# Kernel tuning notes

Hardware: AMD Instinct MI355X
Metric: run time of the kernel (lower is better)

## Reference

```python
import jax, jax.numpy as jnp
import numpy as np

N = 50000      # nodes
E = 640000     # edges
D = 128        # hidden_dim (tower in_dim, towers=1)
DE = 64        # edge_hidden_dim
L = 2          # propagation_depth
AVG_D = 3.5    # avg_d scaler constant
EPS = 1e-5


def setup_inputs() -> dict:
    key = jax.random.key(0)
    ks = jax.random.split(key, 8)
    h = jax.random.normal(ks[0], (N, D), jnp.float32)
    e = jax.random.normal(ks[1], (E, DE), jnp.float32)
    src = jax.random.randint(ks[2], (E,), 0, N, jnp.int32)
    dst = jax.random.randint(ks[3], (E,), 0, N, jnp.int32)
    pre_in = 2 * D + DE            # cat([h_src, h_dst, e])
    post_in = (4 * 3 + 1) * D      # (n_agg * n_scalers + 1) * in_dim
    pre_W = jax.random.normal(ks[4], (L, pre_in, D), jnp.float32) * 0.05
    pre_b = jnp.zeros((L, D), jnp.float32)
    post_W = jax.random.normal(ks[5], (L, post_in, D), jnp.float32) * 0.02
    post_b = jnp.zeros((L, D), jnp.float32)
    mix_W = jax.random.normal(ks[6], (L, D, D), jnp.float32) * 0.05
    mix_b = jnp.zeros((L, D), jnp.float32)
    return {"h": h, "e": e, "src": src, "dst": dst,
            "pre_W": pre_W, "pre_b": pre_b,
            "post_W": post_W, "post_b": post_b,
            "mix_W": mix_W, "mix_b": mix_b}


def reference(h, e, src, dst, pre_W, pre_b, post_W, post_b, mix_W, mix_b):
    n = h.shape[0]
    # in-degree (number of messages per dst node) and scaler coefficients
    deg = jax.ops.segment_sum(jnp.ones((src.shape[0],), h.dtype), dst, num_segments=n)
    deg_c = jnp.maximum(deg, 1.0)[:, None]              # safe divisor for mean
    logd = jnp.log(deg + 1.0)
    amp = (logd / AVG_D)[:, None]                       # amplification scaler
    att = (AVG_D / jnp.maximum(logd, EPS))[:, None]     # attenuation scaler
    has_msg = (deg > 0)[:, None]

    n_layers = pre_W.shape[0]
    for l in range(n_layers):
        # pretrans MLP on edges (1 layer, last_activation='none')
        z2 = jnp.concatenate([h[src], h[dst], e], axis=1)          # [E, 2D+DE]
        m = z2 @ pre_W[l] + pre_b[l]                               # [E, D]
        # multi-aggregator segment reduce over incoming messages per dst
        s = jax.ops.segment_sum(m, dst, num_segments=n)
        s2 = jax.ops.segment_sum(m * m, dst, num_segments=n)
        mean = s / deg_c
        var = jax.nn.relu(s2 / deg_c - mean * mean)
        std = jnp.sqrt(var + EPS)
        mx = jax.ops.segment_max(m, dst, num_segments=n)
        mn = jax.ops.segment_min(m, dst, num_segments=n)
        agg = jnp.concatenate([mean, mx, mn, std], axis=1)         # [N, 4D]
        agg = jnp.where(has_msg, agg, 0.0)                         # zero-degree nodes get no message
        # scalers: identity / amplification / attenuation
        scaled = jnp.concatenate([agg, agg * amp, agg * att], axis=1)  # [N, 12D]
        # posttrans MLP on [h, aggregated] (1 layer, no BN)
        z = jnp.concatenate([h, scaled], axis=1)                   # [N, 13D]
        ht = z @ post_W[l] + post_b[l]                             # [N, D]
        # mixing network + LeakyReLU, residual (in_dim == out_dim)
        ht = jax.nn.leaky_relu(ht @ mix_W[l] + mix_b[l], negative_slope=0.01)
        h = h + ht
    return h
```

## Files before the change

### kernel.cpp

```cpp
#include <hip/hip_runtime.h>

#define NN 50000
#define EE 640000
#define KPRE 320
#define AVGD 3.5f
#define EPSF 1e-5f

typedef unsigned int u32;
typedef unsigned short u16;
typedef __attribute__((ext_vector_type(8))) short short8v;
typedef __attribute__((ext_vector_type(4))) float f32x4;

__device__ __forceinline__ u16 f2bf(float f) {
    u32 u = __float_as_uint(f);
    u32 r = (u + 0x7fffu + ((u >> 16) & 1u)) >> 16;
    return (u16)r;
}
__device__ __forceinline__ float bf2f(u16 b) {
    return __uint_as_float(((u32)b) << 16);
}
__device__ __forceinline__ u32 pack2(float a, float b) {
    return (u32)f2bf(a) | ((u32)f2bf(b) << 16);
}

__device__ __forceinline__ void gload_lds16(const u16* g, u16* l) {
    __builtin_amdgcn_global_load_lds(
        (const __attribute__((address_space(1))) void*)g,
        (__attribute__((address_space(3))) void*)l,
        16, 0, 0);
}


__global__ void deg_kernel(const int* __restrict__ dst, int* __restrict__ deg) {
    int i = blockIdx.x * blockDim.x + threadIdx.x;
    if (i < EE) atomicAdd(&deg[dst[i]], 1);
}

__global__ void scaler_kernel(const int* __restrict__ deg,
                              float* __restrict__ amp, float* __restrict__ att) {
    int i = blockIdx.x * blockDim.x + threadIdx.x;
    if (i < NN) {
        float d = (float)deg[i];
        float logd = logf(d + 1.0f);
        amp[i] = logd / AVGD;
        att[i] = AVGD / fmaxf(logd, EPSF);
    }
}

__global__ void scan_kernel(const int* __restrict__ deg, int* __restrict__ rowstart) {
    __shared__ int wsum[16];
    int lane = threadIdx.x & 63;
    int wid = threadIdx.x >> 6;
    int carry = 0;
    if (threadIdx.x == 0) rowstart[0] = 0;
    for (int base = 0; base < NN; base += 1024) {
        int i = base + threadIdx.x;
        int v = (i < NN) ? deg[i] : 0;
        int x = v;
#pragma unroll
        for (int off = 1; off < 64; off <<= 1) {
            int y = __shfl_up(x, off, 64);
            if (lane >= off) x += y;
        }
        if (lane == 63) wsum[wid] = x;
        __syncthreads();
        if (wid == 0 && lane < 16) {
            int w = wsum[lane];
#pragma unroll
            for (int off = 1; off < 16; off <<= 1) {
                int y = __shfl_up(w, off, 64);
                if (lane >= off) w += y;
            }
            wsum[lane] = w;
        }
        __syncthreads();
        int wofs = (wid > 0) ? wsum[wid - 1] : 0;
        int total = wsum[15];
        if (i < NN) rowstart[i + 1] = carry + wofs + x;
        carry += total;
        __syncthreads();
    }
}

__global__ void fill_kernel(const int* __restrict__ dst, const int* __restrict__ rowstart,
                            int* __restrict__ cursor, int* __restrict__ eid) {
    int i = blockIdx.x * blockDim.x + threadIdx.x;
    if (i < EE) {
        int d = dst[i];
        int pos = rowstart[d] + atomicAdd(&cursor[d], 1);
        eid[pos] = i;
    }
}

__global__ void perm_idx_kernel(const int* __restrict__ eid,
                                const int* __restrict__ src, const int* __restrict__ dst,
                                int* __restrict__ psrc, int* __restrict__ pdst) {
    int p = blockIdx.x * blockDim.x + threadIdx.x;
    if (p < EE) {
        int e = eid[p];
        psrc[p] = src[e];
        pdst[p] = dst[e];
    }
}


__global__ void cvt_h_kernel(const float* __restrict__ h, u16* __restrict__ hb) {
    int i = (blockIdx.x * blockDim.x + threadIdx.x) * 4;
    float4 v = *(const float4*)&h[i];
    uint2 p;
    p.x = pack2(v.x, v.y);
    p.y = pack2(v.z, v.w);
    *(uint2*)&hb[i] = p;
}

__global__ void cvt_ebf_kernel(const float* __restrict__ efeat, const int* __restrict__ eid,
                               u16* __restrict__ ebf) {
    int t = blockIdx.x * blockDim.x + threadIdx.x;
    int p = t >> 3, j = (t & 7) * 8;
    if (p < EE) {
        const float* ep = efeat + (size_t)eid[p] * 64 + j;
        float4 f0 = *(const float4*)ep;
        float4 f1 = *(const float4*)(ep + 4);
        uint4 o;
        o.x = pack2(f0.x, f0.y); o.y = pack2(f0.z, f0.w);
        o.z = pack2(f1.x, f1.y); o.w = pack2(f1.z, f1.w);
        *(uint4*)&ebf[(size_t)p * 64 + j] = o;
    }
}

__global__ void cvt_wt_kernel(const float* __restrict__ W, u16* __restrict__ Wt, int K) {
    int idx = blockIdx.x * blockDim.x + threadIdx.x;
    if (idx < 128 * K) {
        int c = idx / K;
        int k = idx - c * K;
        Wt[idx] = f2bf(W[(size_t)k * 128 + c]);
    }
}

__global__ void cvt_wp_kernel(const float* __restrict__ postW, u16* __restrict__ Wp) {
    int idx = blockIdx.x * blockDim.x + threadIdx.x;
    if (idx < 384 * 640) {
        int c = idx / 640, k = idx - c * 640;
        float v;
        if (c < 128)      v = postW[(size_t)k * 128 + c];
        else if (k < 128) v = 0.f;
        else if (c < 256) v = postW[(size_t)(640 + k - 128) * 128 + (c - 128)];
        else              v = postW[(size_t)(1152 + k - 128) * 128 + (c - 256)];
        Wp[idx] = f2bf(v);
    }
}


__global__ __launch_bounds__(256, 4) void pretrans_mfma(
    const u16* __restrict__ hb, const u16* __restrict__ ebf,
    const int* __restrict__ psrc, const int* __restrict__ pdst,
    const u16* __restrict__ Wt, const float* __restrict__ bias,
    u16* __restrict__ m) {
    __shared__ u16 Bs[2][128][32];
    __shared__ u16 As[2][128][32];
    int t = threadIdx.x;
    int l = t & 63, wid = t >> 6;
    int r = l & 15, g = l >> 4;
    int wr = wid >> 1, wc = wid & 1;
    int bb = blockIdx.x * 128;

    int srow = wid * 16 + (l >> 2);
    int p = l & 3;
    int gs = (p ^ (srow & 3)) * 8;
    int ps1 = psrc[bb + srow], ps2 = psrc[bb + srow + 64];
    int pd1 = pdst[bb + srow], pd2 = pdst[bb + srow + 64];
    u16* ldsB1base[2] = { &Bs[0][wid * 16][0], &Bs[1][wid * 16][0] };
    u16* ldsA1base[2] = { &As[0][wid * 16][0], &As[1][wid * 16][0] };

    f32x4 acc[4][4];
#pragma unroll
    for (int es = 0; es < 4; es++)
#pragma unroll
        for (int cs = 0; cs < 4; cs++) acc[es][cs] = (f32x4)(0.f);

    auto stage = [&](int c, int buf) {
        const u16 *g1, *g2;
        if (c < 8) {
            int kb = (c & 3) * 32;
            int i1 = (c < 4) ? ps1 : pd1;
            int i2 = (c < 4) ? ps2 : pd2;
            g1 = hb + (size_t)i1 * 128 + kb + gs;
            g2 = hb + (size_t)i2 * 128 + kb + gs;
        } else {
            int kb = (c - 8) * 32;
            g1 = ebf + (size_t)(bb + srow) * 64 + kb + gs;
            g2 = ebf + (size_t)(bb + srow + 64) * 64 + kb + gs;
        }
        gload_lds16(g1, ldsB1base[buf]);
        gload_lds16(g2, ldsB1base[buf] + 64 * 32);
        const u16* a1 = Wt + (size_t)srow * KPRE + c * 32 + gs;
        const u16* a2 = Wt + (size_t)(srow + 64) * KPRE + c * 32 + gs;
        gload_lds16(a1, ldsA1base[buf]);
        gload_lds16(a2, ldsA1base[buf] + 64 * 32);
    };

    int sw = (g ^ (r & 3)) * 8;
    stage(0, 0);
#pragma unroll
    for (int c = 0; c < 10; c++) {
        __syncthreads();
        if (c < 9) stage(c + 1, (c + 1) & 1);
        int cb = c & 1;
        short8v bfr[4], afr[4];
#pragma unroll
        for (int es = 0; es < 4; es++)
            bfr[es] = *(const short8v*)&Bs[cb][wr * 64 + es * 16 + r][sw];
#pragma unroll
        for (int cs = 0; cs < 4; cs++)
            afr[cs] = *(const short8v*)&As[cb][wc * 64 + cs * 16 + r][sw];
#pragma unroll
        for (int cs = 0; cs < 4; cs++)
#pragma unroll
            for (int es = 0; es < 4; es++)
                acc[es][cs] = __builtin_amdgcn_mfma_f32_16x16x32_bf16(afr[cs], bfr[es], acc[es][cs], 0, 0, 0);
    }

#pragma unroll
    for (int cs = 0; cs < 4; cs++) {
        int c0 = wc * 64 + cs * 16 + g * 4;
        float4 bi = *(const float4*)&bias[c0];
#pragma unroll
        for (int es = 0; es < 4; es++) {
            size_t gedge = (size_t)bb + wr * 64 + es * 16 + r;
            uint2 pkd;
            pkd.x = pack2(acc[es][cs][0] + bi.x, acc[es][cs][1] + bi.y);
            pkd.y = pack2(acc[es][cs][2] + bi.z, acc[es][cs][3] + bi.w);
            *(uint2*)&m[gedge * 128 + c0] = pkd;
        }
    }
}


__global__ __launch_bounds__(256) void agg_kernel(
    const u16* __restrict__ m, const int* __restrict__ rowstart,
    u16* __restrict__ aggb) {
    int w = blockIdx.x * 4 + (threadIdx.x >> 6);
    if (w >= NN) return;
    int lane = threadIdx.x & 63;
    int beg = rowstart[w], end = rowstart[w + 1];
    float s0 = 0.f, s1 = 0.f, q0 = 0.f, q1 = 0.f;
    float mx0 = -3.402823e38f, mx1 = -3.402823e38f;
    float mn0 = 3.402823e38f, mn1 = 3.402823e38f;
    for (int p = beg; p < end; p++) {
        u32 pk = *(const u32*)&m[(size_t)p * 128 + 2 * lane];
        float v0 = bf2f((u16)(pk & 0xffffu));
        float v1 = bf2f((u16)(pk >> 16));
        s0 += v0; s1 += v1;
        q0 += v0 * v0; q1 += v1 * v1;
        mx0 = fmaxf(mx0, v0); mx1 = fmaxf(mx1, v1);
        mn0 = fminf(mn0, v0); mn1 = fminf(mn1, v1);
    }
    int d = end - beg;
    size_t base = (size_t)w * 512 + 2 * lane;
    if (d > 0) {
        float inv = 1.0f / (float)d;
        float me0 = s0 * inv, me1 = s1 * inv;
        float sd0 = sqrtf(fmaxf(q0 * inv - me0 * me0, 0.f) + EPSF);
        float sd1 = sqrtf(fmaxf(q1 * inv - me1 * me1, 0.f) + EPSF);
        *(u32*)&aggb[base + 0]   = pack2(me0, me1);
        *(u32*)&aggb[base + 128] = pack2(mx0, mx1);
        *(u32*)&aggb[base + 256] = pack2(mn0, mn1);
        *(u32*)&aggb[base + 384] = pack2(sd0, sd1);
    } else {
        *(u32*)&aggb[base + 0]   = 0u;
        *(u32*)&aggb[base + 128] = 0u;
        *(u32*)&aggb[base + 256] = 0u;
        *(u32*)&aggb[base + 384] = 0u;
    }
}


__global__ __launch_bounds__(256, 4) void post_mfma(
    const u16* __restrict__ hb, const u16* __restrict__ aggb,
    const u16* __restrict__ Wp, float* __restrict__ C) {
    __shared__ u16 Bs[2][128][32];
    __shared__ u16 As[2][128][32];
    int t = threadIdx.x;
    int l = t & 63, wid = t >> 6;
    int r = l & 15, g = l >> 4;
    int wr = wid >> 1, wc = wid & 1;
    int nb = blockIdx.x * 128;
    int gset = blockIdx.y;

    int srow = wid * 16 + (l >> 2);
    int p = l & 3;
    int gs = (p ^ (srow & 3)) * 8;
    int n1 = nb + srow;     if (n1 >= NN) n1 = NN - 1;
    int n2 = nb + srow + 64; if (n2 >= NN) n2 = NN - 1;
    u16* ldsB1base[2] = { &Bs[0][wid * 16][0], &Bs[1][wid * 16][0] };
    u16* ldsA1base[2] = { &As[0][wid * 16][0], &As[1][wid * 16][0] };

    f32x4 acc[4][4];
#pragma unroll
    for (int es = 0; es < 4; es++)
#pragma unroll
        for (int cs = 0; cs < 4; cs++) acc[es][cs] = (f32x4)(0.f);

    auto stage = [&](int c, int buf) {
        const u16 *g1, *g2;
        if (c < 4) {
            int kb = c * 32;
            g1 = hb + (size_t)n1 * 128 + kb + gs;
            g2 = hb + (size_t)n2 * 128 + kb + gs;
        } else {
            int kb = (c - 4) * 32;
            g1 = aggb + (size_t)n1 * 512 + kb + gs;
            g2 = aggb + (size_t)n2 * 512 + kb + gs;
        }
        gload_lds16(g1, ldsB1base[buf]);
        gload_lds16(g2, ldsB1base[buf] + 64 * 32);
        const u16* a1 = Wp + (size_t)(gset * 128 + srow) * 640 + c * 32 + gs;
        const u16* a2 = Wp + (size_t)(gset * 128 + srow + 64) * 640 + c * 32 + gs;
        gload_lds16(a1, ldsA1base[buf]);
        gload_lds16(a2, ldsA1base[buf] + 64 * 32);
    };

    int sw = (g ^ (r & 3)) * 8;
    int c0s = (gset > 0) ? 4 : 0;
    stage(c0s, 0);
    for (int c = c0s; c < 20; c++) {
        __syncthreads();
        if (c < 19) stage(c + 1, (c + 1 - c0s) & 1);
        int cb = (c - c0s) & 1;
        short8v bfr[4], afr[4];
#pragma unroll
        for (int es = 0; es < 4; es++)
            bfr[es] = *(const short8v*)&Bs[cb][wr * 64 + es * 16 + r][sw];
#pragma unroll
        for (int cs = 0; cs < 4; cs++)
            afr[cs] = *(const short8v*)&As[cb][wc * 64 + cs * 16 + r][sw];
#pragma unroll
        for (int cs = 0; cs < 4; cs++)
#pragma unroll
            for (int es = 0; es < 4; es++)
                acc[es][cs] = __builtin_amdgcn_mfma_f32_16x16x32_bf16(afr[cs], bfr[es], acc[es][cs], 0, 0, 0);
    }

    float* Cg = C + (size_t)gset * NN * 128;
#pragma unroll
    for (int cs = 0; cs < 4; cs++) {
        int cc = wc * 64 + cs * 16 + g * 4;
#pragma unroll
        for (int es = 0; es < 4; es++) {
            int node = nb + wr * 64 + es * 16 + r;
            if (node < NN) {
                float4 o;
                o.x = acc[es][cs][0]; o.y = acc[es][cs][1];
                o.z = acc[es][cs][2]; o.w = acc[es][cs][3];
                *(float4*)&Cg[(size_t)node * 128 + cc] = o;
            }
        }
    }
}


__global__ __launch_bounds__(256, 3) void mix_mfma(
    const float* __restrict__ C, const float* __restrict__ amp, const float* __restrict__ att,
    const float* __restrict__ postB, const u16* __restrict__ Wt,
    const float* __restrict__ bias, float* __restrict__ h, u16* __restrict__ hb) {
    int l = threadIdx.x & 63;
    int wid = threadIdx.x >> 6;
    int r = l & 15, g = l >> 4;
    int nbase = blockIdx.x * 128 + wid * 32;
    const float* C1 = C + (size_t)NN * 128;
    const float* C2 = C + (size_t)2 * NN * 128;

    int nd[2]; float av[2], tv[2];
#pragma unroll
    for (int es = 0; es < 2; es++) {
        int n2 = nbase + es * 16 + r;
        nd[es] = n2;
        int nc = n2 < NN ? n2 : NN - 1;
        av[es] = amp[nc]; tv[es] = att[nc];
    }

    f32x4 acc[2][8];
#pragma unroll
    for (int es = 0; es < 2; es++)
#pragma unroll
        for (int cs = 0; cs < 8; cs++) acc[es][cs] = (f32x4)(0.f);

#pragma unroll
    for (int ks = 0; ks < 4; ks++) {
        int k0 = ks * 32 + g * 8;
        float4 pb0 = *(const float4*)&postB[k0];
        float4 pb1 = *(const float4*)&postB[k0 + 4];
        short8v b[2];
#pragma unroll
        for (int es = 0; es < 2; es++) {
            int nc = nd[es] < NN ? nd[es] : NN - 1;
            size_t off = (size_t)nc * 128 + k0;
            float4 x0a = *(const float4*)&C[off],  x0b = *(const float4*)&C[off + 4];
            float4 x1a = *(const float4*)&C1[off], x1b = *(const float4*)&C1[off + 4];
            float4 x2a = *(const float4*)&C2[off], x2b = *(const float4*)&C2[off + 4];
            float a2 = av[es], t2 = tv[es];
            float v0 = x0a.x + a2 * x1a.x + t2 * x2a.x + pb0.x;
            float v1 = x0a.y + a2 * x1a.y + t2 * x2a.y + pb0.y;
            float v2 = x0a.z + a2 * x1a.z + t2 * x2a.z + pb0.z;
            float v3 = x0a.w + a2 * x1a.w + t2 * x2a.w + pb0.w;
            float v4 = x0b.x + a2 * x1b.x + t2 * x2b.x + pb1.x;
            float v5 = x0b.y + a2 * x1b.y + t2 * x2b.y + pb1.y;
            float v6 = x0b.z + a2 * x1b.z + t2 * x2b.z + pb1.z;
            float v7 = x0b.w + a2 * x1b.w + t2 * x2b.w + pb1.w;
            short8v bb;
            bb[0] = (short)f2bf(v0); bb[1] = (short)f2bf(v1);
            bb[2] = (short)f2bf(v2); bb[3] = (short)f2bf(v3);
            bb[4] = (short)f2bf(v4); bb[5] = (short)f2bf(v5);
            bb[6] = (short)f2bf(v6); bb[7] = (short)f2bf(v7);
            b[es] = bb;
        }
#pragma unroll
        for (int cs = 0; cs < 8; cs++) {
            short8v a = *(const short8v*)(Wt + (size_t)(cs * 16 + r) * 128 + ks * 32 + g * 8);
            acc[0][cs] = __builtin_amdgcn_mfma_f32_16x16x32_bf16(a, b[0], acc[0][cs], 0, 0, 0);
            acc[1][cs] = __builtin_amdgcn_mfma_f32_16x16x32_bf16(a, b[1], acc[1][cs], 0, 0, 0);
        }
    }

#pragma unroll
    for (int cs = 0; cs < 8; cs++) {
        int c0 = cs * 16 + g * 4;
        float4 bi = *(const float4*)&bias[c0];
#pragma unroll
        for (int es = 0; es < 2; es++) {
            if (nd[es] < NN) {
                float4 v;
                v.x = acc[es][cs][0] + bi.x; v.y = acc[es][cs][1] + bi.y;
                v.z = acc[es][cs][2] + bi.z; v.w = acc[es][cs][3] + bi.w;
                v.x = v.x > 0.f ? v.x : 0.01f * v.x;
                v.y = v.y > 0.f ? v.y : 0.01f * v.y;
                v.z = v.z > 0.f ? v.z : 0.01f * v.z;
                v.w = v.w > 0.f ? v.w : 0.01f * v.w;
                size_t idx = (size_t)nd[es] * 128 + c0;
                float4 old = *(const float4*)&h[idx];
                float4 nw;
                nw.x = old.x + v.x; nw.y = old.y + v.y;
                nw.z = old.z + v.z; nw.w = old.w + v.w;
                *(float4*)&h[idx] = nw;
                uint2 pb;
                pb.x = pack2(nw.x, nw.y);
                pb.y = pack2(nw.z, nw.w);
                *(uint2*)&hb[idx] = pb;
            }
        }
    }
}


extern "C" void kernel_launch(void* const* d_in, const int* in_sizes, int n_in,
                              void* d_out, int out_size, void* d_ws, size_t ws_size,
                              hipStream_t stream) {
    (void)in_sizes; (void)n_in; (void)out_size; (void)ws_size;
    const float* h0    = (const float*)d_in[0];
    const float* efeat = (const float*)d_in[1];
    const int* src     = (const int*)d_in[2];
    const int* dst     = (const int*)d_in[3];
    const float* preW  = (const float*)d_in[4];
    const float* preB  = (const float*)d_in[5];
    const float* postW = (const float*)d_in[6];
    const float* postB = (const float*)d_in[7];
    const float* mixW  = (const float*)d_in[8];
    const float* mixB  = (const float*)d_in[9];
    float* hcur = (float*)d_out;

    char* ws = (char*)d_ws;
    size_t off = 0;
    auto alloc = [&](size_t bytes) {
        void* p = ws + off;
        off += (bytes + 255) & ~(size_t)255;
        return p;
    };
    u16* mbuf    = (u16*)alloc((size_t)EE * 128 * 2);
    u16* ebf     = (u16*)alloc((size_t)EE * 64 * 2);
    u16* aggb    = (u16*)alloc((size_t)NN * 512 * 2);
    u16* hb      = (u16*)alloc((size_t)NN * 128 * 2);
    u16* preWt   = (u16*)alloc((size_t)128 * KPRE * 2);
    u16* Wp      = (u16*)alloc((size_t)384 * 640 * 2);
    u16* mixWt   = (u16*)alloc((size_t)128 * 128 * 2);
    int* eid     = (int*)alloc((size_t)EE * 4);
    int* psrc    = (int*)alloc((size_t)EE * 4);
    int* pdst    = (int*)alloc((size_t)EE * 4);
    int* deg     = (int*)alloc((size_t)NN * 4);
    int* rowstart= (int*)alloc((size_t)(NN + 1) * 4);
    int* cursor  = (int*)alloc((size_t)NN * 4);
    float* amp   = (float*)alloc((size_t)NN * 4);
    float* att   = (float*)alloc((size_t)NN * 4);
    float* C     = (float*)mbuf;

    hipMemsetAsync(deg, 0, (size_t)NN * 4, stream);
    hipMemsetAsync(cursor, 0, (size_t)NN * 4, stream);
    hipMemcpyAsync(hcur, h0, (size_t)NN * 128 * 4, hipMemcpyDeviceToDevice, stream);

    deg_kernel<<<(EE + 255) / 256, 256, 0, stream>>>(dst, deg);
    scaler_kernel<<<(NN + 255) / 256, 256, 0, stream>>>(deg, amp, att);
    scan_kernel<<<1, 1024, 0, stream>>>(deg, rowstart);
    fill_kernel<<<(EE + 255) / 256, 256, 0, stream>>>(dst, rowstart, cursor, eid);
    perm_idx_kernel<<<(EE + 255) / 256, 256, 0, stream>>>(eid, src, dst, psrc, pdst);
    cvt_ebf_kernel<<<(EE * 8 + 255) / 256, 256, 0, stream>>>(efeat, eid, ebf);
    cvt_h_kernel<<<(NN * 128 / 4 + 255) / 256, 256, 0, stream>>>(hcur, hb);

    for (int l = 0; l < 2; l++) {
        cvt_wt_kernel<<<(128 * KPRE + 255) / 256, 256, 0, stream>>>(
            preW + (size_t)l * KPRE * 128, preWt, KPRE);
        cvt_wp_kernel<<<(384 * 640 + 255) / 256, 256, 0, stream>>>(
            postW + (size_t)l * 1664 * 128, Wp);
        cvt_wt_kernel<<<(128 * 128 + 255) / 256, 256, 0, stream>>>(
            mixW + (size_t)l * 128 * 128, mixWt, 128);

        pretrans_mfma<<<EE / 128, 256, 0, stream>>>(
            hb, ebf, psrc, pdst, preWt, preB + (size_t)l * 128, mbuf);
        agg_kernel<<<(NN + 3) / 4, 256, 0, stream>>>(mbuf, rowstart, aggb);
        post_mfma<<<dim3((NN + 127) / 128, 3), 256, 0, stream>>>(hb, aggb, Wp, C);
        mix_mfma<<<(NN + 127) / 128, 256, 0, stream>>>(
            C, amp, att, postB, mixWt, mixB + (size_t)l * 128, hcur, hb);
    }
}
```

Measured before the change: 1.020 ms.

## Stage GEMM epilogues through swizzled LDS and store post-GEMM partials as bf16

Both pretrans and post GEMM epilogues now write their tiles into shared memory with an XOR swizzle, then emit full-row coalesced 16-byte stores instead of scattered 8/16-byte per-lane stores. The post GEMM partial outputs C are stored as bf16 rather than fp32, which halves their write and read traffic. The post bias is folded into the gset==0 partial and mix reads bf16. The launch-bound hint for occupancy is raised to 5. The cost is extra bf16 rounding of intermediate partials before the amp/att scaling, plus two more barriers per block.

Result: faster. 987.7 us (-3.2%).

```diff
diff --git a/kernel.cpp b/kernel.cpp
--- a/kernel.cpp
+++ b/kernel.cpp
@@ -151,13 +151,14 @@
 }
 
 
-__global__ __launch_bounds__(256, 4) void pretrans_mfma(
+__global__ __launch_bounds__(256, 5) void pretrans_mfma(
     const u16* __restrict__ hb, const u16* __restrict__ ebf,
     const int* __restrict__ psrc, const int* __restrict__ pdst,
     const u16* __restrict__ Wt, const float* __restrict__ bias,
     u16* __restrict__ m) {
-    __shared__ u16 Bs[2][128][32];
-    __shared__ u16 As[2][128][32];
+    __shared__ u16 smem[16384];
+    u16* BsP = smem;
+    u16* AsP = smem + 8192;
     int t = threadIdx.x;
     int l = t & 63, wid = t >> 6;
     int r = l & 15, g = l >> 4;
@@ -169,8 +170,6 @@
     int gs = (p ^ (srow & 3)) * 8;
     int ps1 = psrc[bb + srow], ps2 = psrc[bb + srow + 64];
     int pd1 = pdst[bb + srow], pd2 = pdst[bb + srow + 64];
-    u16* ldsB1base[2] = { &Bs[0][wid * 16][0], &Bs[1][wid * 16][0] };
-    u16* ldsA1base[2] = { &As[0][wid * 16][0], &As[1][wid * 16][0] };
 
     f32x4 acc[4][4];
 #pragma unroll
@@ -191,12 +190,14 @@
             g1 = ebf + (size_t)(bb + srow) * 64 + kb + gs;
             g2 = ebf + (size_t)(bb + srow + 64) * 64 + kb + gs;
         }
-        gload_lds16(g1, ldsB1base[buf]);
-        gload_lds16(g2, ldsB1base[buf] + 64 * 32);
+        u16* bB = &BsP[((size_t)buf * 128 + wid * 16) * 32];
+        gload_lds16(g1, bB);
+        gload_lds16(g2, bB + 64 * 32);
         const u16* a1 = Wt + (size_t)srow * KPRE + c * 32 + gs;
         const u16* a2 = Wt + (size_t)(srow + 64) * KPRE + c * 32 + gs;
-        gload_lds16(a1, ldsA1base[buf]);
-        gload_lds16(a2, ldsA1base[buf] + 64 * 32);
+        u16* bA = &AsP[((size_t)buf * 128 + wid * 16) * 32];
+        gload_lds16(a1, bA);
+        gload_lds16(a2, bA + 64 * 32);
     };
 
     int sw = (g ^ (r & 3)) * 8;
@@ -209,10 +210,10 @@
         short8v bfr[4], afr[4];
 #pragma unroll
         for (int es = 0; es < 4; es++)
-            bfr[es] = *(const short8v*)&Bs[cb][wr * 64 + es * 16 + r][sw];
+            bfr[es] = *(const short8v*)&BsP[((size_t)cb * 128 + wr * 64 + es * 16 + r) * 32 + sw];
 #pragma unroll
         for (int cs = 0; cs < 4; cs++)
-            afr[cs] = *(const short8v*)&As[cb][wc * 64 + cs * 16 + r][sw];
+            afr[cs] = *(const short8v*)&AsP[((size_t)cb * 128 + wc * 64 + cs * 16 + r) * 32 + sw];
 #pragma unroll
         for (int cs = 0; cs < 4; cs++)
 #pragma unroll
@@ -220,18 +221,30 @@
                 acc[es][cs] = __builtin_amdgcn_mfma_f32_16x16x32_bf16(afr[cs], bfr[es], acc[es][cs], 0, 0, 0);
     }
 
+    __syncthreads();
 #pragma unroll
     for (int cs = 0; cs < 4; cs++) {
         int c0 = wc * 64 + cs * 16 + g * 4;
         float4 bi = *(const float4*)&bias[c0];
 #pragma unroll
         for (int es = 0; es < 4; es++) {
-            size_t gedge = (size_t)bb + wr * 64 + es * 16 + r;
+            int row = wr * 64 + es * 16 + r;
+            int cbyte = (c0 * 2) ^ ((row & 7) << 4);
             uint2 pkd;
             pkd.x = pack2(acc[es][cs][0] + bi.x, acc[es][cs][1] + bi.y);
             pkd.y = pack2(acc[es][cs][2] + bi.z, acc[es][cs][3] + bi.w);
-            *(uint2*)&m[gedge * 128 + c0] = pkd;
-        }
+            *(uint2*)((char*)smem + row * 256 + cbyte) = pkd;
+        }
+    }
+    __syncthreads();
+#pragma unroll
+    for (int it = 0; it < 8; it++) {
+        int idx = it * 256 + t;
+        int row = idx >> 4;
+        int cb2 = (idx & 15) * 16;
+        int swz = cb2 ^ ((row & 7) << 4);
+        uint4 v = *(const uint4*)((const char*)smem + row * 256 + swz);
+        *(uint4*)((char*)(m + (size_t)(bb + row) * 128) + cb2) = v;
     }
 }
 
@@ -275,11 +288,13 @@
 }
 
 
-__global__ __launch_bounds__(256, 4) void post_mfma(
+__global__ __launch_bounds__(256, 5) void post_mfma(
     const u16* __restrict__ hb, const u16* __restrict__ aggb,
-    const u16* __restrict__ Wp, float* __restrict__ C) {
-    __shared__ u16 Bs[2][128][32];
-    __shared__ u16 As[2][128][32];
+    const u16* __restrict__ Wp, const float* __restrict__ postB,
+    u16* __restrict__ C) {
+    __shared__ u16 smem[16384];
+    u16* BsP = smem;
+    u16* AsP = smem + 8192;
     int t = threadIdx.x;
     int l = t & 63, wid = t >> 6;
     int r = l & 15, g = l >> 4;
@@ -290,10 +305,8 @@
     int srow = wid * 16 + (l >> 2);
     int p = l & 3;
     int gs = (p ^ (srow & 3)) * 8;
-    int n1 = nb + srow;     if (n1 >= NN) n1 = NN - 1;
+    int n1 = nb + srow;      if (n1 >= NN) n1 = NN - 1;
     int n2 = nb + srow + 64; if (n2 >= NN) n2 = NN - 1;
-    u16* ldsB1base[2] = { &Bs[0][wid * 16][0], &Bs[1][wid * 16][0] };
-    u16* ldsA1base[2] = { &As[0][wid * 16][0], &As[1][wid * 16][0] };
 
     f32x4 acc[4][4];
 #pragma unroll
@@ -312,12 +325,14 @@
             g1 = aggb + (size_t)n1 * 512 + kb + gs;
             g2 = aggb + (size_t)n2 * 512 + kb + gs;
         }
-        gload_lds16(g1, ldsB1base[buf]);
-        gload_lds16(g2, ldsB1base[buf] + 64 * 32);
+        u16* bB = &BsP[((size_t)buf * 128 + wid * 16) * 32];
+        gload_lds16(g1, bB);
+        gload_lds16(g2, bB + 64 * 32);
         const u16* a1 = Wp + (size_t)(gset * 128 + srow) * 640 + c * 32 + gs;
         const u16* a2 = Wp + (size_t)(gset * 128 + srow + 64) * 640 + c * 32 + gs;
-        gload_lds16(a1, ldsA1base[buf]);
-        gload_lds16(a2, ldsA1base[buf] + 64 * 32);
+        u16* bA = &AsP[((size_t)buf * 128 + wid * 16) * 32];
+        gload_lds16(a1, bA);
+        gload_lds16(a2, bA + 64 * 32);
     };
 
     int sw = (g ^ (r & 3)) * 8;
@@ -330,10 +345,10 @@
         short8v bfr[4], afr[4];
 #pragma unroll
         for (int es = 0; es < 4; es++)
-            bfr[es] = *(const short8v*)&Bs[cb][wr * 64 + es * 16 + r][sw];
+            bfr[es] = *(const short8v*)&BsP[((size_t)cb * 128 + wr * 64 + es * 16 + r) * 32 + sw];
 #pragma unroll
         for (int cs = 0; cs < 4; cs++)
-            afr[cs] = *(const short8v*)&As[cb][wc * 64 + cs * 16 + r][sw];
+            afr[cs] = *(const short8v*)&AsP[((size_t)cb * 128 + wc * 64 + cs * 16 + r) * 32 + sw];
 #pragma unroll
         for (int cs = 0; cs < 4; cs++)
 #pragma unroll
@@ -341,34 +356,48 @@
                 acc[es][cs] = __builtin_amdgcn_mfma_f32_16x16x32_bf16(afr[cs], bfr[es], acc[es][cs], 0, 0, 0);
     }
 
-    float* Cg = C + (size_t)gset * NN * 128;
+    __syncthreads();
 #pragma unroll
     for (int cs = 0; cs < 4; cs++) {
-        int cc = wc * 64 + cs * 16 + g * 4;
+        int c0 = wc * 64 + cs * 16 + g * 4;
+        float4 bi = make_float4(0.f, 0.f, 0.f, 0.f);
+        if (gset == 0) bi = *(const float4*)&postB[c0];
 #pragma unroll
         for (int es = 0; es < 4; es++) {
-            int node = nb + wr * 64 + es * 16 + r;
-            if (node < NN) {
-                float4 o;
-                o.x = acc[es][cs][0]; o.y = acc[es][cs][1];
-                o.z = acc[es][cs][2]; o.w = acc[es][cs][3];
-                *(float4*)&Cg[(size_t)node * 128 + cc] = o;
-            }
+            int row = wr * 64 + es * 16 + r;
+            int cbyte = (c0 * 2) ^ ((row & 7) << 4);
+            uint2 pkd;
+            pkd.x = pack2(acc[es][cs][0] + bi.x, acc[es][cs][1] + bi.y);
+            pkd.y = pack2(acc[es][cs][2] + bi.z, acc[es][cs][3] + bi.w);
+            *(uint2*)((char*)smem + row * 256 + cbyte) = pkd;
+        }
+    }
+    __syncthreads();
+    u16* Cg = C + (size_t)gset * NN * 128;
+#pragma unroll
+    for (int it = 0; it < 8; it++) {
+        int idx = it * 256 + t;
+        int row = idx >> 4;
+        int cb2 = (idx & 15) * 16;
+        int swz = cb2 ^ ((row & 7) << 4);
+        if (nb + row < NN) {
+            uint4 v = *(const uint4*)((const char*)smem + row * 256 + swz);
+            *(uint4*)((char*)(Cg + (size_t)(nb + row) * 128) + cb2) = v;
         }
     }
 }
 
 
 __global__ __launch_bounds__(256, 3) void mix_mfma(
-    const float* __restrict__ C, const float* __restrict__ amp, const float* __restrict__ att,
-    const float* __restrict__ postB, const u16* __restrict__ Wt,
-    const float* __restrict__ bias, float* __restrict__ h, u16* __restrict__ hb) {
+    const u16* __restrict__ C, const float* __restrict__ amp, const float* __restrict__ att,
+    const u16* __restrict__ Wt, const float* __restrict__ bias,
+    float* __restrict__ h, u16* __restrict__ hb) {
     int l = threadIdx.x & 63;
     int wid = threadIdx.x >> 6;
     int r = l & 15, g = l >> 4;
     int nbase = blockIdx.x * 128 + wid * 32;
-    const float* C1 = C + (size_t)NN * 128;
-    const float* C2 = C + (size_t)2 * NN * 128;
+    const u16* C1 = C + (size_t)NN * 128;
+    const u16* C2 = C + (size_t)2 * NN * 128;
 
     int nd[2]; float av[2], tv[2];
 #pragma unroll
@@ -388,31 +417,22 @@
 #pragma unroll
     for (int ks = 0; ks < 4; ks++) {
         int k0 = ks * 32 + g * 8;
-        float4 pb0 = *(const float4*)&postB[k0];
-        float4 pb1 = *(const float4*)&postB[k0 + 4];
         short8v b[2];
 #pragma unroll
         for (int es = 0; es < 2; es++) {
             int nc = nd[es] < NN ? nd[es] : NN - 1;
             size_t off = (size_t)nc * 128 + k0;
-            float4 x0a = *(const float4*)&C[off],  x0b = *(const float4*)&C[off + 4];
-            float4 x1a = *(const float4*)&C1[off], x1b = *(const float4*)&C1[off + 4];
-            float4 x2a = *(const float4*)&C2[off], x2b = *(const float4*)&C2[off + 4];
+            short8v s0 = *(const short8v*)&C[off];
+            short8v s1 = *(const short8v*)&C1[off];
+            short8v s2 = *(const short8v*)&C2[off];
             float a2 = av[es], t2 = tv[es];
-            float v0 = x0a.x + a2 * x1a.x + t2 * x2a.x + pb0.x;
-            float v1 = x0a.y + a2 * x1a.y + t2 * x2a.y + pb0.y;
-            float v2 = x0a.z + a2 * x1a.z + t2 * x2a.z + pb0.z;
-            float v3 = x0a.w + a2 * x1a.w + t2 * x2a.w + pb0.w;
-            float v4 = x0b.x + a2 * x1b.x + t2 * x2b.x + pb1.x;
-            float v5 = x0b.y + a2 * x1b.y + t2 * x2b.y + pb1.y;
-            float v6 = x0b.z + a2 * x1b.z + t2 * x2b.z + pb1.z;
-            float v7 = x0b.w + a2 * x1b.w + t2 * x2b.w + pb1.w;
-            short8v bb;
-            bb[0] = (short)f2bf(v0); bb[1] = (short)f2bf(v1);
-            bb[2] = (short)f2bf(v2); bb[3] = (short)f2bf(v3);
-            bb[4] = (short)f2bf(v4); bb[5] = (short)f2bf(v5);
-            bb[6] = (short)f2bf(v6); bb[7] = (short)f2bf(v7);
-            b[es] = bb;
+            short8v bbv;
+#pragma unroll
+            for (int j = 0; j < 8; j++) {
+                float v = bf2f((u16)s0[j]) + a2 * bf2f((u16)s1[j]) + t2 * bf2f((u16)s2[j]);
+                bbv[j] = (short)f2bf(v);
+            }
+            b[es] = bbv;
         }
 #pragma unroll
         for (int cs = 0; cs < 8; cs++) {
@@ -490,7 +510,7 @@
     int* cursor  = (int*)alloc((size_t)NN * 4);
     float* amp   = (float*)alloc((size_t)NN * 4);
     float* att   = (float*)alloc((size_t)NN * 4);
-    float* C     = (float*)mbuf;
+    u16* Cb      = (u16*)mbuf;
 
     hipMemsetAsync(deg, 0, (size_t)NN * 4, stream);
     hipMemsetAsync(cursor, 0, (size_t)NN * 4, stream);
@@ -515,8 +535,9 @@
         pretrans_mfma<<<EE / 128, 256, 0, stream>>>(
             hb, ebf, psrc, pdst, preWt, preB + (size_t)l * 128, mbuf);
         agg_kernel<<<(NN + 3) / 4, 256, 0, stream>>>(mbuf, rowstart, aggb);
-        post_mfma<<<dim3((NN + 127) / 128, 3), 256, 0, stream>>>(hb, aggb, Wp, C);
+        post_mfma<<<dim3((NN + 127) / 128, 3), 256, 0, stream>>>(
+            hb, aggb, Wp, postB + (size_t)l * 128, Cb);
         mix_mfma<<<(NN + 127) / 128, 256, 0, stream>>>(
-            C, amp, att, postB, mixWt, mixB + (size_t)l * 128, hcur, hb);
-    }
-}
+            Cb, amp, att, mixWt, mixB + (size_t)l * 128, hcur, hb);
+    }
+}
```
